# Performance work log

Measured on AMD Instinct MI355X. Metric: run time of the kernel, lower is better.

The kernel has to match this reference:

```python
import jax, jax.numpy as jnp
import numpy as np

IN_FEATURES = 4096  # 64*64


def setup_inputs() -> dict:
    key = jax.random.key(0)
    kx, k0, k1, k2, k3 = jax.random.split(key, 5)
    u = lambda k, s: jax.random.uniform(k, s, jnp.float32, -0.1, 0.1)
    return {
        "x": jax.random.normal(kx, (8192, 4096), jnp.float32),
        "core0": u(k0, (1, 64, 16)),
        "core1": u(k1, (16, 64, 16)),
        "core2": u(k2, (16, 64, 16)),
        "core3": u(k3, (16, 64, 1)),
    }


def tt_to_matrix(cores, in_features):
    # Sequentially contract TT cores: cores[i] has shape (r_{i-1}, n_i, r_i).
    # Running result: (prod_of_dims_so_far, r_i)
    W = cores[0].reshape(cores[0].shape[1], cores[0].shape[2])  # (n0, r1)
    for c in cores[1:]:
        # (P, r) x (r, n, r') -> (P*n, r')
        W = jnp.einsum("pr,rns->pns", W, c).reshape(-1, c.shape[2])
    return W.reshape(in_features, -1)  # (in_features, out_features)


def reference(x, core0, core1, core2, core3):
    W = tt_to_matrix((core0, core1, core2, core3), IN_FEATURES)  # (4096, 4096)
    return jnp.matmul(x, W)
```

## Files before the change

kernel.cpp:

```cpp
#include <hip/hip_runtime.h>

#define ROWS 8192
#define KDIM 4096
#define NDIM 4096

typedef float f32x4 __attribute__((ext_vector_type(4)));


__device__ inline f32x4 fma4(float s, f32x4 w, f32x4 a) {
    a.x = fmaf(s, w.x, a.x);
    a.y = fmaf(s, w.y, a.y);
    a.z = fmaf(s, w.z, a.z);
    a.w = fmaf(s, w.w, a.w);
    return a;
}
__device__ inline f32x4 shfl_xor4(f32x4 v, int m) {
    v.x = __shfl_xor(v.x, m, 64);
    v.y = __shfl_xor(v.y, m, 64);
    v.z = __shfl_xor(v.z, m, 64);
    v.w = __shfl_xor(v.w, m, 64);
    return v;
}

__global__ __launch_bounds__(256) void tt_prep(
    const float* __restrict__ c0, const float* __restrict__ c1,
    const float* __restrict__ c2, const float* __restrict__ c3,
    float* __restrict__ w01, float* __restrict__ w23)
{
    int gid = blockIdx.x * 256 + threadIdx.x;
    if (gid < 65536) {
        int p = gid >> 4, r2 = gid & 15;
        int n0 = p >> 6, n1 = p & 63;
        float s = 0.f;
        #pragma unroll
        for (int r1 = 0; r1 < 16; ++r1)
            s = fmaf(c0[n0 * 16 + r1], c1[(r1 * 64 + n1) * 16 + r2], s);
        w01[gid] = s;
    } else {
        int g = gid - 65536;
        int r2 = g >> 12, j = g & 4095;
        int n2 = j >> 6, n3 = j & 63;
        float s = 0.f;
        #pragma unroll
        for (int r3 = 0; r3 < 16; ++r3)
            s = fmaf(c2[(r2 * 64 + n2) * 16 + r3], c3[r3 * 64 + n3], s);
        w23[g] = s;
    }
}

__global__ __launch_bounds__(256) void tt_fused(
    const float* __restrict__ x, const float* __restrict__ w01,
    const float* __restrict__ w23, float* __restrict__ out)
{
    __shared__ __align__(16) float tsp[4][8][16];
    __shared__ __align__(16) float ts[8][16];
    const int t = threadIdx.x;
    const int lane = t & 63;
    const int wv = t >> 6;
    const int q = lane & 3;
    const int klane = lane >> 2;
    const int row0 = blockIdx.x * 8;
    const int k0 = wv * 1024;

    const float* xb = x + (size_t)row0 * KDIM + k0;
    const float* wb = w01 + (size_t)k0 * 16;

    f32x4 acc[8];
    #pragma unroll
    for (int r = 0; r < 8; ++r) acc[r] = (f32x4)(0.f);

    #pragma unroll 2
    for (int it = 0; it < 1024 / 64; ++it) {
        const int kk0 = it * 64 + klane * 4;
        f32x4 wq[4];
        #pragma unroll
        for (int kk = 0; kk < 4; ++kk)
            wq[kk] = *(const f32x4*)&wb[(size_t)(kk0 + kk) * 16 + q * 4];
        f32x4 xv[8];
        #pragma unroll
        for (int r = 0; r < 8; ++r)
            xv[r] = *(const f32x4*)&xb[(size_t)r * KDIM + kk0];
        #pragma unroll
        for (int kk = 0; kk < 4; ++kk)
            #pragma unroll
            for (int r = 0; r < 8; ++r)
                acc[r] = fma4(xv[r][kk], wq[kk], acc[r]);
    }

    const bool b5 = lane & 32, b4 = lane & 16, b3 = lane & 8;
    f32x4 s1[4];
    #pragma unroll
    for (int j = 0; j < 4; ++j) {
        f32x4 send = b5 ? acc[j] : acc[4 + j];
        f32x4 keep = b5 ? acc[4 + j] : acc[j];
        s1[j] = keep + shfl_xor4(send, 32);
    }
    f32x4 s2[2];
    #pragma unroll
    for (int j = 0; j < 2; ++j) {
        f32x4 send = b4 ? s1[j] : s1[2 + j];
        f32x4 keep = b4 ? s1[2 + j] : s1[j];
        s2[j] = keep + shfl_xor4(send, 16);
    }
    f32x4 s3;
    {
        f32x4 send = b3 ? s2[0] : s2[1];
        f32x4 keep = b3 ? s2[1] : s2[0];
        s3 = keep + shfl_xor4(send, 8);
    }
    s3 += shfl_xor4(s3, 4);

    if ((lane & 4) == 0) {
        int row = (lane >> 3) & 7;
        *(f32x4*)&tsp[wv][row][q * 4] = s3;
    }
    __syncthreads();

    if (t < 128) {
        int row = t >> 4, r = t & 15;
        ts[row][r] = tsp[0][row][r] + tsp[1][row][r]
                   + tsp[2][row][r] + tsp[3][row][r];
    }
    __syncthreads();

    const size_t obase = (size_t)row0 * NDIM;
    #pragma unroll 1
    for (int jt = 0; jt < 4; ++jt) {
        const int j0 = jt * 1024 + t * 4;
        f32x4 w[16];
        #pragma unroll
        for (int r = 0; r < 16; ++r)
            w[r] = *(const f32x4*)&w23[r * NDIM + j0];
        #pragma unroll 2
        for (int row = 0; row < 8; ++row) {
            const f32x4* trp = (const f32x4*)&ts[row][0];
            f32x4 t0 = trp[0], t1 = trp[1], t2 = trp[2], t3 = trp[3];
            f32x4 a = (f32x4)(0.f);
            a = fma4(t0.x, w[0],  a); a = fma4(t0.y, w[1],  a);
            a = fma4(t0.z, w[2],  a); a = fma4(t0.w, w[3],  a);
            a = fma4(t1.x, w[4],  a); a = fma4(t1.y, w[5],  a);
            a = fma4(t1.z, w[6],  a); a = fma4(t1.w, w[7],  a);
            a = fma4(t2.x, w[8],  a); a = fma4(t2.y, w[9],  a);
            a = fma4(t2.z, w[10], a); a = fma4(t2.w, w[11], a);
            a = fma4(t3.x, w[12], a); a = fma4(t3.y, w[13], a);
            a = fma4(t3.z, w[14], a); a = fma4(t3.w, w[15], a);
            __builtin_nontemporal_store(a,
                (f32x4*)&out[obase + (size_t)row * NDIM + j0]);
        }
    }
}

extern "C" void kernel_launch(void* const* d_in, const int* in_sizes, int n_in,
                              void* d_out, int out_size, void* d_ws, size_t ws_size,
                              hipStream_t stream) {
    const float* x  = (const float*)d_in[0];
    const float* c0 = (const float*)d_in[1];
    const float* c1 = (const float*)d_in[2];
    const float* c2 = (const float*)d_in[3];
    const float* c3 = (const float*)d_in[4];
    float* out = (float*)d_out;

    float* w01 = (float*)d_ws;
    float* w23 = w01 + 65536;

    tt_prep<<<512, 256, 0, stream>>>(c0, c1, c2, c3, w01, w23);
    tt_fused<<<1024, 256, 0, stream>>>(x, w01, w23, out);
}
```

Baseline: 59.98 us.

## Overlap second row-group projection with first group's output writes via warp specialization

Each block now handles 16 rows with 512 threads. It reduces the first 8 rows across all 8 waves. It then splits the waves: four compute the x·W01 reduction for the second 8 rows while the other four write the first group's output through W23. The aim is to overlap the x read stream with the large output write stream inside one block instead of running them in separate phases. The cost is fewer blocks, more syncs, and an unbalanced split of work between the waves.

```diff
diff --git a/kernel.cpp b/kernel.cpp
--- a/kernel.cpp
+++ b/kernel.cpp
@@ -48,29 +48,16 @@
     }
 }
 
-__global__ __launch_bounds__(256) void tt_fused(
-    const float* __restrict__ x, const float* __restrict__ w01,
-    const float* __restrict__ w23, float* __restrict__ out)
-{
-    __shared__ __align__(16) float tsp[4][8][16];
-    __shared__ __align__(16) float ts[8][16];
-    const int t = threadIdx.x;
-    const int lane = t & 63;
-    const int wv = t >> 6;
-    const int q = lane & 3;
-    const int klane = lane >> 2;
-    const int row0 = blockIdx.x * 8;
-    const int k0 = wv * 1024;
-
-    const float* xb = x + (size_t)row0 * KDIM + k0;
-    const float* wb = w01 + (size_t)k0 * 16;
-
+__device__ __forceinline__ f32x4 p1_engine(
+    const float* __restrict__ xb, const float* __restrict__ wb,
+    int nit, int lane, int q, int klane)
+{
     f32x4 acc[8];
     #pragma unroll
     for (int r = 0; r < 8; ++r) acc[r] = (f32x4)(0.f);
 
     #pragma unroll 2
-    for (int it = 0; it < 1024 / 64; ++it) {
+    for (int it = 0; it < nit; ++it) {
         const int kk0 = it * 64 + klane * 4;
         f32x4 wq[4];
         #pragma unroll
@@ -109,44 +96,102 @@
         s3 = keep + shfl_xor4(send, 8);
     }
     s3 += shfl_xor4(s3, 4);
-
-    if ((lane & 4) == 0) {
-        int row = (lane >> 3) & 7;
-        *(f32x4*)&tsp[wv][row][q * 4] = s3;
-    }
-    __syncthreads();
-
+    return s3;
+}
+
+__device__ __forceinline__ void p2_rows(
+    const float (*ts)[16], const f32x4* w, float* __restrict__ out,
+    size_t obase, int j0)
+{
+    #pragma unroll 2
+    for (int row = 0; row < 8; ++row) {
+        const f32x4* trp = (const f32x4*)&ts[row][0];
+        f32x4 t0 = trp[0], t1 = trp[1], t2 = trp[2], t3 = trp[3];
+        f32x4 a = (f32x4)(0.f);
+        a = fma4(t0.x, w[0],  a); a = fma4(t0.y, w[1],  a);
+        a = fma4(t0.z, w[2],  a); a = fma4(t0.w, w[3],  a);
+        a = fma4(t1.x, w[4],  a); a = fma4(t1.y, w[5],  a);
+        a = fma4(t1.z, w[6],  a); a = fma4(t1.w, w[7],  a);
+        a = fma4(t2.x, w[8],  a); a = fma4(t2.y, w[9],  a);
+        a = fma4(t2.z, w[10], a); a = fma4(t2.w, w[11], a);
+        a = fma4(t3.x, w[12], a); a = fma4(t3.y, w[13], a);
+        a = fma4(t3.z, w[14], a); a = fma4(t3.w, w[15], a);
+        __builtin_nontemporal_store(a,
+            (f32x4*)&out[obase + (size_t)row * NDIM + j0]);
+    }
+}
+
+__global__ __launch_bounds__(512) void tt_fused(
+    const float* __restrict__ x, const float* __restrict__ w01,
+    const float* __restrict__ w23, float* __restrict__ out)
+{
+    __shared__ __align__(16) float tsp[8][8][16];
+    __shared__ __align__(16) float tsA[8][16];
+    __shared__ __align__(16) float tsB[8][16];
+    const int t = threadIdx.x;
+    const int lane = t & 63;
+    const int wv = t >> 6;
+    const int q = lane & 3;
+    const int klane = lane >> 2;
+    const int rowA = blockIdx.x * 16;
+    const int rowB = rowA + 8;
+    const size_t obaseA = (size_t)rowA * NDIM;
+    const size_t obaseB = (size_t)rowB * NDIM;
+
+    {
+        const int k0 = wv * 512;
+        f32x4 s3 = p1_engine(x + (size_t)rowA * KDIM + k0,
+                             w01 + (size_t)k0 * 16, 8, lane, q, klane);
+        if ((lane & 4) == 0) {
+            int row = (lane >> 3) & 7;
+            *(f32x4*)&tsp[wv][row][q * 4] = s3;
+        }
+    }
+    __syncthreads();
     if (t < 128) {
         int row = t >> 4, r = t & 15;
-        ts[row][r] = tsp[0][row][r] + tsp[1][row][r]
-                   + tsp[2][row][r] + tsp[3][row][r];
-    }
-    __syncthreads();
-
-    const size_t obase = (size_t)row0 * NDIM;
+        tsA[row][r] = tsp[0][row][r] + tsp[1][row][r] + tsp[2][row][r]
+                    + tsp[3][row][r] + tsp[4][row][r] + tsp[5][row][r]
+                    + tsp[6][row][r] + tsp[7][row][r];
+    }
+    __syncthreads();
+
+    if (wv < 4) {
+        const int k0 = wv * 1024;
+        f32x4 s3 = p1_engine(x + (size_t)rowB * KDIM + k0,
+                             w01 + (size_t)k0 * 16, 16, lane, q, klane);
+        if ((lane & 4) == 0) {
+            int row = (lane >> 3) & 7;
+            *(f32x4*)&tsp[wv][row][q * 4] = s3;
+        }
+    } else {
+        const int t2 = t - 256;
+        #pragma unroll 1
+        for (int jt = 0; jt < 4; ++jt) {
+            const int j0 = jt * 1024 + t2 * 4;
+            f32x4 w[16];
+            #pragma unroll
+            for (int r = 0; r < 16; ++r)
+                w[r] = *(const f32x4*)&w23[r * NDIM + j0];
+            p2_rows(tsA, w, out, obaseA, j0);
+        }
+    }
+    __syncthreads();
+    if (t < 128) {
+        int row = t >> 4, r = t & 15;
+        tsB[row][r] = tsp[0][row][r] + tsp[1][row][r]
+                    + tsp[2][row][r] + tsp[3][row][r];
+    }
+    __syncthreads();
+
     #pragma unroll 1
-    for (int jt = 0; jt < 4; ++jt) {
-        const int j0 = jt * 1024 + t * 4;
+    for (int jt = 0; jt < 2; ++jt) {
+        const int j0 = jt * 2048 + t * 4;
         f32x4 w[16];
         #pragma unroll
         for (int r = 0; r < 16; ++r)
             w[r] = *(const f32x4*)&w23[r * NDIM + j0];
-        #pragma unroll 2
-        for (int row = 0; row < 8; ++row) {
-            const f32x4* trp = (const f32x4*)&ts[row][0];
-            f32x4 t0 = trp[0], t1 = trp[1], t2 = trp[2], t3 = trp[3];
-            f32x4 a = (f32x4)(0.f);
-            a = fma4(t0.x, w[0],  a); a = fma4(t0.y, w[1],  a);
-            a = fma4(t0.z, w[2],  a); a = fma4(t0.w, w[3],  a);
-            a = fma4(t1.x, w[4],  a); a = fma4(t1.y, w[5],  a);
-            a = fma4(t1.z, w[6],  a); a = fma4(t1.w, w[7],  a);
-            a = fma4(t2.x, w[8],  a); a = fma4(t2.y, w[9],  a);
-            a = fma4(t2.z, w[10], a); a = fma4(t2.w, w[11], a);
-            a = fma4(t3.x, w[12], a); a = fma4(t3.y, w[13], a);
-            a = fma4(t3.z, w[14], a); a = fma4(t3.w, w[15], a);
-            __builtin_nontemporal_store(a,
-                (f32x4*)&out[obase + (size_t)row * NDIM + j0]);
-        }
+        p2_rows(tsB, w, out, obaseB, j0);
     }
 }
 
@@ -164,5 +209,5 @@
     float* w23 = w01 + 65536;
 
     tt_prep<<<512, 256, 0, stream>>>(c0, c1, c2, c3, w01, w23);
-    tt_fused<<<1024, 256, 0, stream>>>(x, w01, w23, out);
-}
+    tt_fused<<<512, 512, 0, stream>>>(x, w01, w23, out);
+}
```

Result: slower. 65.50 us (+9.2%).
